# Kernel tuning notes

Measured on AMD Instinct MI355X. Metric: run time of the kernel, lower is better.

## Reference

```python
import jax, jax.numpy as jnp
import numpy as np

ALPHA = 0.2          # LeakyReLU negative slope
NEG_BIG = -9e15      # mask fill value from the original code
N, IN_F, OUT_F = 8192, 128, 64


def setup_inputs() -> dict:
    key = jax.random.key(0)
    k1, k2, k3, k4 = jax.random.split(key, 4)
    h = jax.random.normal(k1, (N, IN_F), dtype=jnp.float32)
    adj = jax.random.randint(k2, (N, N), 0, 2, dtype=jnp.int32)
    W = jax.random.normal(k3, (IN_F, OUT_F), dtype=jnp.float32) * 0.1
    a = jax.random.normal(k4, (2 * OUT_F, 1), dtype=jnp.float32) * 0.1
    return {"h": h, "adj": adj, "W": W, "a": a}


def reference(h, adj, W, a):
    # Wh: [N, F]
    Wh = h @ W
    # e_ij = leakyrelu([Wh_i ; Wh_j] . a) = leakyrelu(Wh_i.a1 + Wh_j.a2)
    # (identical math to the original NxNx2F concat, without materializing it)
    a1 = a[:OUT_F, 0]   # [F]
    a2 = a[OUT_F:, 0]   # [F]
    s1 = Wh @ a1        # [N]
    s2 = Wh @ a2        # [N]
    e = jax.nn.leaky_relu(s1[:, None] + s2[None, :], negative_slope=ALPHA)  # [N, N]
    e = jnp.where(adj > 0, e, jnp.float32(NEG_BIG))
    attention = jax.nn.softmax(e, axis=1)
    # dropout is identity at inference (training=False)
    h_prime = attention @ Wh  # [N, F]
    return jax.nn.elu(h_prime)  # concat=True -> elu
```

## Files before the change

kernel.cpp:

```cpp
#include <hip/hip_runtime.h>
#include <hip/hip_bf16.h>

#define N 8192
#define IN_F 128
#define OUT_F 64
#define LRELU_ALPHA 0.2f
#define SPLIT 4
#define RPB 64
#define CPB 2048
#define WIN 512
#define NWIN 4
#define TSTR 129

typedef __attribute__((ext_vector_type(8))) short short8;
typedef __attribute__((ext_vector_type(4))) short short4v;
typedef __attribute__((ext_vector_type(4))) float float4v;
typedef __attribute__((ext_vector_type(4))) unsigned short ushortx4;

__device__ __forceinline__ unsigned short bf16_bits(float x) {
  unsigned u = __builtin_bit_cast(unsigned, x);
  u += 0x7fffu + ((u >> 16) & 1u);
  return (unsigned short)(u >> 16);
}

__global__ __launch_bounds__(256) void prep_kernel(
    const float* __restrict__ h, const float* __restrict__ W,
    const float* __restrict__ a, float* __restrict__ s1,
    float* __restrict__ s2, unsigned short* __restrict__ whT) {
  const int tid = threadIdx.x;
  const int row = blockIdx.x * 4 + (tid >> 6);
  const int k = tid & 63;
  const float* hr = h + row * IN_F;
  float acc = 0.f;
#pragma unroll 8
  for (int c = 0; c < IN_F; ++c) acc = fmaf(hr[c], W[c * OUT_F + k], acc);
  whT[(long)k * N + row] = bf16_bits(acc);
  float p1 = acc * a[k];
  float p2 = acc * a[OUT_F + k];
#pragma unroll
  for (int off = 32; off > 0; off >>= 1) {
    p1 += __shfl_xor(p1, off);
    p2 += __shfl_xor(p2, off);
  }
  if (k == 0) { s1[row] = p1; s2[row] = p2; }
}

__global__ __launch_bounds__(256) void repack_kernel(
    const unsigned short* __restrict__ whT, unsigned short* __restrict__ whF) {
  const int f = blockIdx.x * 256 + threadIdx.x;
  const int lane = f & 63, tt = (f >> 6) & 3, c = f >> 8;
  const int r16 = lane & 15, quad = lane >> 4;
  const short8 v = *(const short8*)(whT + (long)(tt * 16 + r16) * N + c * 32 + quad * 8);
  *(short8*)(whF + (long)f * 8) = v;
}

__device__ __forceinline__ float p_half(unsigned short* dst, int4 av,
                                        float4 s2v, float s1w) {
  float e0 = s1w + s2v.x; e0 = fmaxf(e0, LRELU_ALPHA * e0);
  float e1 = s1w + s2v.y; e1 = fmaxf(e1, LRELU_ALPHA * e1);
  float e2 = s1w + s2v.z; e2 = fmaxf(e2, LRELU_ALPHA * e2);
  float e3 = s1w + s2v.w; e3 = fmaxf(e3, LRELU_ALPHA * e3);
  const float p0 = av.x > 0 ? __expf(e0) : 0.f;
  const float p1 = av.y > 0 ? __expf(e1) : 0.f;
  const float p2 = av.z > 0 ? __expf(e2) : 0.f;
  const float p3 = av.w > 0 ? __expf(e3) : 0.f;
  ushortx4 pk = {bf16_bits(p0), bf16_bits(p1), bf16_bits(p2), bf16_bits(p3)};
  *(ushortx4*)dst = pk;
  return (p0 + p1) + (p2 + p3);
}

__global__ __launch_bounds__(512, 4) void gat_kernel(
    const int* __restrict__ adj, const float* __restrict__ s1,
    const float* __restrict__ s2, const unsigned short* __restrict__ whF,
    float* __restrict__ pacc, float* __restrict__ pl) {
  __shared__ __align__(16) unsigned short ptile[RPB * TSTR * 4];
  __shared__ __align__(16) float s2l[CPB];
  const int tid = threadIdx.x;
  const int w = tid >> 6, L = tid & 63;
  const int r16 = L & 15, quad = L >> 4;
  const int rb = blockIdx.x, cs = blockIdx.y;
  const int row0 = rb * RPB;
  const int colbase = cs * CPB;

  *(float4*)(s2l + tid * 4) = *(const float4*)(s2 + colbase + tid * 4);

  float s1r[8];
#pragma unroll
  for (int j = 0; j < 8; ++j) s1r[j] = s1[row0 + w * 8 + j];

  float lsum[8] = {0.f, 0.f, 0.f, 0.f, 0.f, 0.f, 0.f, 0.f};
  float4v acc[4][4];
#pragma unroll
  for (int rt = 0; rt < 4; ++rt)
#pragma unroll
    for (int dt = 0; dt < 4; ++dt) acc[rt][dt] = (float4v){0.f, 0.f, 0.f, 0.f};

  __syncthreads();

  for (int it = 0; it < NWIN; ++it) {
    const int c0 = it * WIN + L * 4;
    const float4 sva = *(const float4*)(s2l + c0);
    const float4 svb = *(const float4*)(s2l + c0 + 256);
#pragma unroll
    for (int half = 0; half < 2; ++half) {
      int4 ja[4], jb[4];
#pragma unroll
      for (int j2 = 0; j2 < 4; ++j2) {
        const int r = half * 4 + j2;
        const long arow = (long)(row0 + w * 8 + r) * N + colbase + c0;
        ja[j2] = *(const int4*)(adj + arow);
        jb[j2] = *(const int4*)(adj + arow + 256);
      }
#pragma unroll
      for (int j2 = 0; j2 < 4; ++j2) {
        const int r = half * 4 + j2;
        unsigned short* rowp = ptile + (w * 8 + r) * TSTR * 4;
        lsum[r] += p_half(rowp + L * 4, ja[j2], sva, s1r[r]);
        lsum[r] += p_half(rowp + (64 + L) * 4, jb[j2], svb, s1r[r]);
      }
    }
    __syncthreads();
#pragma unroll
    for (int ci = 0; ci < 2; ++ci) {
      const int c = w + ci * 8;
      const unsigned short* bp =
          whF + ((long)(cs * 64 + it * 16 + c) * 256 + L) * 8;
      const short8 b0 = *(const short8*)(bp);
      const short8 b1 = *(const short8*)(bp + 512);
      const short8 b2 = *(const short8*)(bp + 1024);
      const short8 b3 = *(const short8*)(bp + 1536);
#pragma unroll
      for (int rt = 0; rt < 4; ++rt) {
        const int g = (rt * 16 + r16) * TSTR + c * 8 + quad * 2;
        const short4v alo = *(const short4v*)(ptile + g * 4);
        const short4v ahi = *(const short4v*)(ptile + g * 4 + 4);
        const short8 afrag =
            __builtin_shufflevector(alo, ahi, 0, 1, 2, 3, 4, 5, 6, 7);
        acc[rt][0] = __builtin_amdgcn_mfma_f32_16x16x32_bf16(afrag, b0, acc[rt][0], 0, 0, 0);
        acc[rt][1] = __builtin_amdgcn_mfma_f32_16x16x32_bf16(afrag, b1, acc[rt][1], 0, 0, 0);
        acc[rt][2] = __builtin_amdgcn_mfma_f32_16x16x32_bf16(afrag, b2, acc[rt][2], 0, 0, 0);
        acc[rt][3] = __builtin_amdgcn_mfma_f32_16x16x32_bf16(afrag, b3, acc[rt][3], 0, 0, 0);
      }
    }
    __syncthreads();
  }

#pragma unroll
  for (int j = 0; j < 8; ++j) {
    float v = lsum[j];
#pragma unroll
    for (int off = 1; off < 64; off <<= 1) v += __shfl_xor(v, off);
    if (L == 0) pl[(long)cs * N + row0 + w * 8 + j] = v;
  }

  float* M = (float*)ptile;
  if (w >= 4) {
    float* S = M + (w - 4) * 4096;
#pragma unroll
    for (int rt = 0; rt < 4; ++rt)
#pragma unroll
      for (int dt = 0; dt < 4; ++dt)
#pragma unroll
        for (int reg = 0; reg < 4; ++reg)
          S[(rt * 16 + quad * 4 + reg) * 64 + dt * 16 + r16] = acc[rt][dt][reg];
  }
  __syncthreads();
  if (w < 4) {
    float* S = M + w * 4096;
#pragma unroll
    for (int rt = 0; rt < 4; ++rt)
#pragma unroll
      for (int dt = 0; dt < 4; ++dt)
#pragma unroll
        for (int reg = 0; reg < 4; ++reg)
          S[(rt * 16 + quad * 4 + reg) * 64 + dt * 16 + r16] += acc[rt][dt][reg];
  }
  __syncthreads();
#pragma unroll
  for (int o = tid; o < 1024; o += 512) {
    const int r = o >> 4, k4 = (o & 15) * 4;
    float4 v0 = *(const float4*)(M + 0 * 4096 + r * 64 + k4);
    const float4 v1 = *(const float4*)(M + 1 * 4096 + r * 64 + k4);
    const float4 v2 = *(const float4*)(M + 2 * 4096 + r * 64 + k4);
    const float4 v3 = *(const float4*)(M + 3 * 4096 + r * 64 + k4);
    v0.x += v1.x + v2.x + v3.x;
    v0.y += v1.y + v2.y + v3.y;
    v0.z += v1.z + v2.z + v3.z;
    v0.w += v1.w + v2.w + v3.w;
    *(float4*)(pacc + ((long)cs * N + row0 + r) * OUT_F + k4) = v0;
  }
}

__global__ __launch_bounds__(256) void merge_kernel(
    const float* __restrict__ pacc, const float* __restrict__ pl,
    float* __restrict__ out) {
  const int idx = blockIdx.x * 256 + threadIdx.x;
  const int r = idx >> 4;
  const int k4 = (idx & 15) * 4;
  float4 S = {0.f, 0.f, 0.f, 0.f};
  float Lx = 0.f;
#pragma unroll
  for (int c = 0; c < SPLIT; ++c) {
    const float4 p = *(const float4*)(pacc + ((long)c * N + r) * OUT_F + k4);
    S.x += p.x; S.y += p.y; S.z += p.z; S.w += p.w;
    Lx += pl[(long)c * N + r];
  }
  const float inv = 1.f / Lx;
  float v[4] = {S.x * inv, S.y * inv, S.z * inv, S.w * inv};
  float4 o;
  o.x = v[0] > 0.f ? v[0] : expm1f(v[0]);
  o.y = v[1] > 0.f ? v[1] : expm1f(v[1]);
  o.z = v[2] > 0.f ? v[2] : expm1f(v[2]);
  o.w = v[3] > 0.f ? v[3] : expm1f(v[3]);
  *(float4*)(out + (long)r * OUT_F + k4) = o;
}

extern "C" void kernel_launch(void* const* d_in, const int* in_sizes, int n_in,
                              void* d_out, int out_size, void* d_ws, size_t ws_size,
                              hipStream_t stream) {
  const float* h = (const float*)d_in[0];
  const int* adj = (const int*)d_in[1];
  const float* W = (const float*)d_in[2];
  const float* a = (const float*)d_in[3];
  float* out = (float*)d_out;

  float* s1 = (float*)d_ws;
  float* s2 = s1 + N;
  unsigned short* whT = (unsigned short*)(s2 + N);
  unsigned short* whF = whT + (long)OUT_F * N;
  float* pacc = (float*)(whF + (long)OUT_F * N);
  float* pl = pacc + (long)SPLIT * N * OUT_F;

  prep_kernel<<<N / 4, 256, 0, stream>>>(h, W, a, s1, s2, whT);
  repack_kernel<<<N * OUT_F / 8 / 256, 256, 0, stream>>>(whT, whF);
  gat_kernel<<<dim3(N / RPB, SPLIT), 512, 0, stream>>>(adj, s1, s2, whF, pacc, pl);
  merge_kernel<<<N * OUT_F / 4 / 256, 256, 0, stream>>>(pacc, pl, out);
}
```

Before: 416.8 us.

## Pre-pack adjacency into per-wave bitmasks before the attention kernel

```diff
diff --git a/kernel.cpp b/kernel.cpp
--- a/kernel.cpp
+++ b/kernel.cpp
@@ -16,6 +16,7 @@
 typedef __attribute__((ext_vector_type(4))) short short4v;
 typedef __attribute__((ext_vector_type(4))) float float4v;
 typedef __attribute__((ext_vector_type(4))) unsigned short ushortx4;
+typedef unsigned long long u64;
 
 __device__ __forceinline__ unsigned short bf16_bits(float x) {
   unsigned u = __builtin_bit_cast(unsigned, x);
@@ -54,23 +55,47 @@
   *(short8*)(whF + (long)f * 8) = v;
 }
 
-__device__ __forceinline__ float p_half(unsigned short* dst, int4 av,
-                                        float4 s2v, float s1w) {
+__global__ __launch_bounds__(256) void pack_kernel(
+    const int* __restrict__ adj, u64* __restrict__ pk) {
+  const int tid = threadIdx.x;
+  const int w = tid >> 6, L = tid & 63;
+  const int row = blockIdx.x * 4 + w;
+  const int* rp = adj + (long)row * N;
+  u64* dst = pk + (long)row * 128;
+#pragma unroll 4
+  for (int cc = 0; cc < 32; ++cc) {
+    const int4 a = *(const int4*)(rp + cc * 256 + L * 4);
+    const u64 b0 = __ballot(a.x > 0);
+    const u64 b1 = __ballot(a.y > 0);
+    const u64 b2 = __ballot(a.z > 0);
+    const u64 b3 = __ballot(a.w > 0);
+    if (L == 0) {
+      dst[cc * 4 + 0] = b0;
+      dst[cc * 4 + 1] = b1;
+      dst[cc * 4 + 2] = b2;
+      dst[cc * 4 + 3] = b3;
+    }
+  }
+}
+
+__device__ __forceinline__ float p_half(unsigned short* dst, u64 q0, u64 q1,
+                                        u64 q2, u64 q3, float4 s2v, float s1w,
+                                        int L) {
   float e0 = s1w + s2v.x; e0 = fmaxf(e0, LRELU_ALPHA * e0);
   float e1 = s1w + s2v.y; e1 = fmaxf(e1, LRELU_ALPHA * e1);
   float e2 = s1w + s2v.z; e2 = fmaxf(e2, LRELU_ALPHA * e2);
   float e3 = s1w + s2v.w; e3 = fmaxf(e3, LRELU_ALPHA * e3);
-  const float p0 = av.x > 0 ? __expf(e0) : 0.f;
-  const float p1 = av.y > 0 ? __expf(e1) : 0.f;
-  const float p2 = av.z > 0 ? __expf(e2) : 0.f;
-  const float p3 = av.w > 0 ? __expf(e3) : 0.f;
-  ushortx4 pk = {bf16_bits(p0), bf16_bits(p1), bf16_bits(p2), bf16_bits(p3)};
-  *(ushortx4*)dst = pk;
+  const float p0 = ((q0 >> L) & 1) ? __expf(e0) : 0.f;
+  const float p1 = ((q1 >> L) & 1) ? __expf(e1) : 0.f;
+  const float p2 = ((q2 >> L) & 1) ? __expf(e2) : 0.f;
+  const float p3 = ((q3 >> L) & 1) ? __expf(e3) : 0.f;
+  ushortx4 pkv = {bf16_bits(p0), bf16_bits(p1), bf16_bits(p2), bf16_bits(p3)};
+  *(ushortx4*)dst = pkv;
   return (p0 + p1) + (p2 + p3);
 }
 
 __global__ __launch_bounds__(512, 4) void gat_kernel(
-    const int* __restrict__ adj, const float* __restrict__ s1,
+    const u64* __restrict__ pk, const float* __restrict__ s1,
     const float* __restrict__ s2, const unsigned short* __restrict__ whF,
     float* __restrict__ pacc, float* __restrict__ pl) {
   __shared__ __align__(16) unsigned short ptile[RPB * TSTR * 4];
@@ -102,22 +127,15 @@
     const float4 sva = *(const float4*)(s2l + c0);
     const float4 svb = *(const float4*)(s2l + c0 + 256);
 #pragma unroll
-    for (int half = 0; half < 2; ++half) {
-      int4 ja[4], jb[4];
-#pragma unroll
-      for (int j2 = 0; j2 < 4; ++j2) {
-        const int r = half * 4 + j2;
-        const long arow = (long)(row0 + w * 8 + r) * N + colbase + c0;
-        ja[j2] = *(const int4*)(adj + arow);
-        jb[j2] = *(const int4*)(adj + arow + 256);
-      }
-#pragma unroll
-      for (int j2 = 0; j2 < 4; ++j2) {
-        const int r = half * 4 + j2;
-        unsigned short* rowp = ptile + (w * 8 + r) * TSTR * 4;
-        lsum[r] += p_half(rowp + L * 4, ja[j2], sva, s1r[r]);
-        lsum[r] += p_half(rowp + (64 + L) * 4, jb[j2], svb, s1r[r]);
-      }
+    for (int r = 0; r < 8; ++r) {
+      const u64* mp = pk + (long)(row0 + w * 8 + r) * 128 + (cs * 8 + it * 2) * 4;
+      const ulonglong2 qa = *(const ulonglong2*)(mp);
+      const ulonglong2 qb = *(const ulonglong2*)(mp + 2);
+      const ulonglong2 qc = *(const ulonglong2*)(mp + 4);
+      const ulonglong2 qd = *(const ulonglong2*)(mp + 6);
+      unsigned short* rowp = ptile + (w * 8 + r) * TSTR * 4;
+      lsum[r] += p_half(rowp + L * 4, qa.x, qa.y, qb.x, qb.y, sva, s1r[r], L);
+      lsum[r] += p_half(rowp + (64 + L) * 4, qc.x, qc.y, qd.x, qd.y, svb, s1r[r], L);
     }
     __syncthreads();
 #pragma unroll
@@ -230,9 +248,11 @@
   unsigned short* whF = whT + (long)OUT_F * N;
   float* pacc = (float*)(whF + (long)OUT_F * N);
   float* pl = pacc + (long)SPLIT * N * OUT_F;
+  u64* pk = (u64*)(pl + (long)SPLIT * N);
 
   prep_kernel<<<N / 4, 256, 0, stream>>>(h, W, a, s1, s2, whT);
   repack_kernel<<<N * OUT_F / 8 / 256, 256, 0, stream>>>(whT, whF);
-  gat_kernel<<<dim3(N / RPB, SPLIT), 512, 0, stream>>>(adj, s1, s2, whF, pacc, pl);
+  pack_kernel<<<N / 4, 256, 0, stream>>>(adj, pk);
+  gat_kernel<<<dim3(N / RPB, SPLIT), 512, 0, stream>>>(pk, s1, s2, whF, pacc, pl);
   merge_kernel<<<N * OUT_F / 4 / 256, 256, 0, stream>>>(pacc, pl, out);
 }
```

After: 463.7 us. 11.2% more time.
